# Kernel tuning notes

Measured on AMD Instinct MI355X. Metric: run time of the kernel, lower is better.

The kernel has to match this reference:

```python
import jax, jax.numpy as jnp
import numpy as np

EMB = 1024
HEADS = 16
HEAD_DIM = EMB // HEADS
SCALE = 1.0 / np.sqrt(HEAD_DIM)


def setup_inputs() -> dict:
    key = jax.random.key(0)
    ks = jax.random.split(key, 11)
    B, L, E = 4, 2048, EMB
    s = 1.0 / np.sqrt(E)
    inp = {
        "Q": jax.random.normal(ks[0], (B, L, E), jnp.float32),
        "K": jax.random.normal(ks[1], (B, L, E), jnp.float32),
        "V": jax.random.normal(ks[2], (B, L, E), jnp.float32),
        "WQ": jax.random.normal(ks[3], (E, E), jnp.float32) * s,
        "bQ": jax.random.normal(ks[4], (E,), jnp.float32) * s,
        "WK": jax.random.normal(ks[5], (E, E), jnp.float32) * s,
        "bK": jax.random.normal(ks[6], (E,), jnp.float32) * s,
        "WV": jax.random.normal(ks[7], (E, E), jnp.float32) * s,
        "bV": jax.random.normal(ks[8], (E,), jnp.float32) * s,
        "WO": jax.random.normal(ks[9], (E, E), jnp.float32) * s,
        "bO": jax.random.normal(ks[10], (E,), jnp.float32) * s,
    }
    return inp


def reference(Q, K, V, WQ, bQ, WK, bK, WV, bV, WO, bO):
    B, L, E = Q.shape
    # linear projections (torch Linear stores W as [out,in]; here W is [in,out])
    q = Q @ WQ + bQ
    k = K @ WK + bK
    v = V @ WV + bV
    # split heads: [B, H, L, D]
    q = q.reshape(B, L, HEADS, HEAD_DIM).transpose(0, 2, 1, 3)
    k = k.reshape(B, L, HEADS, HEAD_DIM).transpose(0, 2, 1, 3)
    v = v.reshape(B, L, HEADS, HEAD_DIM).transpose(0, 2, 1, 3)
    scores = jnp.einsum("bhqd,bhkd->bhqk", q, k) * SCALE
    # causal mask (mask=True): -inf above diagonal
    causal = jnp.tril(jnp.ones((L, L), dtype=bool))
    scores = jnp.where(causal, scores, -jnp.inf)
    probs = jax.nn.softmax(scores, axis=-1)
    out = jnp.einsum("bhqk,bhkd->bhqd", probs, v)  # [B,H,L,D]
    out = out.transpose(0, 2, 1, 3).reshape(B, L, E)  # concat heads
    return out @ WO + bO
```

## Files before the change

kernel.cpp:

```cpp
#include <hip/hip_runtime.h>
#include <hip/hip_bf16.h>

#define BB 4
#define HH 16
#define LL 2048
#define DD 64
#define EE 1024
#define MM (BB*LL)
#define SCL 0.125f
#define L2E 1.44269504f

using bf16   = __hip_bfloat16;
using bf16x8 = __attribute__((ext_vector_type(8))) __bf16;
using s16x4  = __attribute__((ext_vector_type(4))) short;
using f32x4  = __attribute__((ext_vector_type(4))) float;
using u32x4  = __attribute__((ext_vector_type(4))) unsigned int;
typedef unsigned int u32;

__device__ __forceinline__ bf16x8 ld8(const bf16* p){ return *(const bf16x8*)p; }
__device__ __forceinline__ bf16x8 ld8(const float* p){
  u32x4 a = *(const u32x4*)p;
  u32x4 b = *(const u32x4*)(p + 4);
  union { bf16x8 v; unsigned short s[8]; } r;
#pragma unroll
  for (int i = 0; i < 4; i++) r.s[i]     = (unsigned short)((a[i] + 0x7FFFu + ((a[i] >> 16) & 1u)) >> 16);
#pragma unroll
  for (int i = 0; i < 4; i++) r.s[i + 4] = (unsigned short)((b[i] + 0x7FFFu + ((b[i] >> 16) & 1u)) >> 16);
  return r.v;
}
__device__ __forceinline__ float ldf(const bf16* p){ return __bfloat162float(*p); }
__device__ __forceinline__ float ldf(const float* p){ return *p; }
__device__ __forceinline__ bf16 to_b(bf16 v){ return v; }
__device__ __forceinline__ bf16 to_b(float v){ return __float2bfloat16(v); }

__device__ __forceinline__ void async16(const bf16* g, bf16* l) {
  __builtin_amdgcn_global_load_lds((const __attribute__((address_space(1))) u32*)g,
                                   (__attribute__((address_space(3))) u32*)l, 16, 0, 0);
}

__global__ __launch_bounds__(256) void detect_dtype(const unsigned int* __restrict__ w,
                                                    int* __restrict__ flag) {
  __shared__ int cnt[256];
  int tid = threadIdx.x;
  int c = 0;
  for (int i = 0; i < 16; i++) {
    unsigned u = w[tid * 16 + i];
    unsigned e = (u >> 7) & 0xFF;
    c += (e >= 100 && e <= 140) ? 1 : 0;
  }
  cnt[tid] = c;
  __syncthreads();
  for (int s = 128; s > 0; s >>= 1) {
    if (tid < s) cnt[tid] += cnt[tid + s];
    __syncthreads();
  }
  if (tid == 0) *flag = (cnt[0] > 2048) ? 1 : 0;
}

__global__ __launch_bounds__(256) void convert_in(
    const void* __restrict__ X0, const void* __restrict__ X1, const void* __restrict__ X2,
    bf16* __restrict__ Y0, bf16* __restrict__ Y1, bf16* __restrict__ Y2,
    const int* __restrict__ flag) {
  int z = blockIdx.z;
  const void* X = (z == 0) ? X0 : (z == 1) ? X1 : X2;
  bf16* Y       = (z == 0) ? Y0 : (z == 1) ? Y1 : Y2;
  size_t idx = ((size_t)blockIdx.x * 256 + threadIdx.x) * 8;
  if (*flag) *(bf16x8*)(Y + idx) = *(const bf16x8*)((const bf16*)X + idx);
  else       *(bf16x8*)(Y + idx) = ld8((const float*)X + idx);
}

template<typename T>
__device__ __forceinline__ void tr_body(const T* __restrict__ W, bf16* __restrict__ Wt,
                                        bf16 (*t)[33]) {
  int tx = threadIdx.x, ty = threadIdx.y;
  int x = blockIdx.x * 32 + tx;
  for (int r = 0; r < 4; r++)
    t[ty + r * 8][tx] = to_b(W[(blockIdx.y * 32 + ty + r * 8) * EE + x]);
  __syncthreads();
  int x2 = blockIdx.y * 32 + tx;
  for (int r = 0; r < 4; r++)
    Wt[(blockIdx.x * 32 + ty + r * 8) * EE + x2] = t[tx][ty + r * 8];
}

__global__ __launch_bounds__(256) void transpose_w4(
    const void* __restrict__ W0, const void* __restrict__ W1,
    const void* __restrict__ W2, const void* __restrict__ W3,
    bf16* __restrict__ T0, bf16* __restrict__ T1,
    bf16* __restrict__ T2, bf16* __restrict__ T3,
    const int* __restrict__ flag) {
  __shared__ bf16 t[32][33];
  int z = blockIdx.z;
  const void* W = (z == 0) ? W0 : (z == 1) ? W1 : (z == 2) ? W2 : W3;
  bf16* Wt      = (z == 0) ? T0 : (z == 1) ? T1 : (z == 2) ? T2 : T3;
  if (*flag) tr_body<bf16>((const bf16*)W, Wt, t);
  else       tr_body<float>((const float*)W, Wt, t);
}

template<typename TIO>
__device__ void gemm_body(const bf16* __restrict__ A, const bf16* __restrict__ Bt,
                          const TIO* __restrict__ bias, void* __restrict__ Cv,
                          int mode, bf16* As, bf16* Bs) {
  constexpr int K = EE;
  int tid = threadIdx.x;
  int lane = tid & 63, w = tid >> 6;
  int l16 = lane & 15, quad = lane >> 4;
  int linear = blockIdx.x + 8 * blockIdx.y;
  int xcd = linear & 7;
  int slot = linear >> 3;
  int m0 = (xcd * 8 + (slot & 7)) * 128;
  int n0 = (slot >> 3) * 128;
  int mw = (w & 1) * 64;
  int nw = (w >> 1) * 64;
  int lr = lane >> 3;
  int x7 = l16 & 7;

  f32x4 acc[4][4] = {};

  for (int k0 = 0; k0 < K; k0 += 64) {
    __syncthreads();
#pragma unroll
    for (int s = 0; s < 4; s++) {
      int R = w * 32 + s * 8;
      int r = R + lr;
      int gc = ((lane & 7) ^ (r & 7)) * 8;
      async16(A  + (size_t)(m0 + r) * K + k0 + gc, As + R * 64);
      async16(Bt + (size_t)(n0 + r) * K + k0 + gc, Bs + R * 64);
    }
    __syncthreads();
#pragma unroll
    for (int ks = 0; ks < 2; ks++) {
      bf16x8 af[4], bfr[4];
#pragma unroll
      for (int t = 0; t < 4; t++) {
        af[t]  = *(const bf16x8*)(As + (mw + t * 16 + l16) * 64 + ((ks * 4 + quad) ^ x7) * 8);
        bfr[t] = *(const bf16x8*)(Bs + (nw + t * 16 + l16) * 64 + ((ks * 4 + quad) ^ x7) * 8);
      }
#pragma unroll
      for (int mt = 0; mt < 4; mt++)
#pragma unroll
        for (int nt = 0; nt < 4; nt++)
          acc[mt][nt] = __builtin_amdgcn_mfma_f32_16x16x32_bf16(af[mt], bfr[nt], acc[mt][nt], 0, 0, 0);
    }
  }

#pragma unroll
  for (int nt = 0; nt < 4; nt++) {
    int col = n0 + nw + nt * 16 + l16;
    float bv = ldf(bias + col);
    int hh = col >> 6, d = col & 63;
#pragma unroll
    for (int mt = 0; mt < 4; mt++) {
      f32x4 v = acc[mt][nt];
      int rowb = m0 + mw + mt * 16 + quad * 4;
      if (mode == 0) {
#pragma unroll
        for (int i = 0; i < 4; i++)
          ((bf16*)Cv)[(size_t)(rowb + i) * EE + col] = __float2bfloat16(v[i] + bv);
      } else if (mode == 3) {
#pragma unroll
        for (int i = 0; i < 4; i++) {
          float val = v[i] + bv;
          if constexpr (__is_same(TIO, bf16))
            ((bf16*)Cv)[(size_t)(rowb + i) * EE + col] = __float2bfloat16(val);
          else
            ((float*)Cv)[(size_t)(rowb + i) * EE + col] = val;
        }
      } else {
        int b = rowb >> 11, l0 = rowb & 2047;
        union { s16x4 p; bf16 e[4]; } u;
#pragma unroll
        for (int i = 0; i < 4; i++) u.e[i] = __float2bfloat16(v[i] + bv);
        *(s16x4*)((bf16*)Cv + ((size_t)(b * HH + hh) * DD + d) * LL + l0) = u.p;
      }
    }
  }
}

__global__ __launch_bounds__(256) void qkv_gemm(
    const bf16* __restrict__ Qc, const bf16* __restrict__ Kc, const bf16* __restrict__ Vc,
    const bf16* __restrict__ WQt, const bf16* __restrict__ WKt, const bf16* __restrict__ WVt,
    const void* __restrict__ bQ, const void* __restrict__ bK, const void* __restrict__ bV,
    bf16* __restrict__ qo, bf16* __restrict__ ko, bf16* __restrict__ vo,
    const int* __restrict__ flag) {
  __shared__ __align__(16) bf16 As[128 * 64];
  __shared__ __align__(16) bf16 Bs[128 * 64];
  int z = blockIdx.z;
  const bf16* A    = (z == 0) ? Qc  : (z == 1) ? Kc  : Vc;
  const bf16* Bt   = (z == 0) ? WQt : (z == 1) ? WKt : WVt;
  const void* bb   = (z == 0) ? bQ  : (z == 1) ? bK  : bV;
  bf16* C          = (z == 0) ? qo  : (z == 1) ? ko  : vo;
  int mode = (z == 2) ? 2 : 0;
  if (*flag) gemm_body<bf16>(A, Bt, (const bf16*)bb, C, mode, As, Bs);
  else       gemm_body<float>(A, Bt, (const float*)bb, C, mode, As, Bs);
}

__global__ __launch_bounds__(256) void out_gemm(const bf16* __restrict__ A,
                                                const bf16* __restrict__ WOt,
                                                const void* __restrict__ bO,
                                                void* __restrict__ C,
                                                const int* __restrict__ flag) {
  __shared__ __align__(16) bf16 As[128 * 64];
  __shared__ __align__(16) bf16 Bs[128 * 64];
  if (*flag) gemm_body<bf16>(A, WOt, (const bf16*)bO, C, 3, As, Bs);
  else       gemm_body<float>(A, WOt, (const float*)bO, C, 3, As, Bs);
}

__global__ __launch_bounds__(256) void attn(const bf16* __restrict__ qg,
                                            const bf16* __restrict__ kg,
                                            const bf16* __restrict__ vg,
                                            bf16* __restrict__ outg) {
  __shared__ __align__(16) bf16 Ks[2][64 * 64];
  __shared__ __align__(16) bf16 Vs[2][64 * 64];
  int linear = blockIdx.x + 16 * blockIdx.y;
  int xcd = linear & 7;
  int slot = linear >> 3;
  int bh = xcd * 8 + (slot & 7);
  int pb = slot >> 3;
  int tid = threadIdx.x;
  int w = tid >> 6, lane = tid & 63, l16 = lane & 15, quad = lane >> 4;
  int b = bh >> 4, hh = bh & 15;

  const bf16* qp = qg + (size_t)b * LL * EE + hh * DD;
  const bf16* kp = kg + (size_t)b * LL * EE + hh * DD;
  const bf16* vp = vg + (size_t)bh * DD * LL;
  const f32x4 z4 = {};
  int x7 = l16 & 7;

  for (int half = 0; half < 2; half++) {
    int tile = half ? (31 - pb) : pb;
    int qrow0 = tile * 64 + w * 16;
    int q = qrow0 + l16;
    bf16x8 bq0 = *(const bf16x8*)(qp + (size_t)q * EE + quad * 8);
    bf16x8 bq1 = *(const bf16x8*)(qp + (size_t)q * EE + 32 + quad * 8);

    float m = -1.0e30f, l = 0.f;
    f32x4 o[4] = {};
    int kend = tile + 1;

    __syncthreads();
    {
      int kbase = 0;
#pragma unroll
      for (int t = 0; t < 2; t++) {
        int R = w * 16 + t * 8;
        int r = R + (lane >> 3);
        int gb = (lane & 7) ^ (r & 7);
        async16(kp + (size_t)(kbase + r) * EE + gb * 8, &Ks[0][R * 64]);
        async16(vp + (size_t)r * LL + kbase + gb * 8, &Vs[0][R * 64]);
      }
    }

    for (int kb = 0; kb < kend; kb++) {
      int kbase = kb * 64;
      __syncthreads();
      if (kb + 1 < kend) {
        int nb = (kb + 1) & 1;
        int nbase = kbase + 64;
#pragma unroll
        for (int t = 0; t < 2; t++) {
          int R = w * 16 + t * 8;
          int r = R + (lane >> 3);
          int gb = (lane & 7) ^ (r & 7);
          async16(kp + (size_t)(nbase + r) * EE + gb * 8, &Ks[nb][R * 64]);
          async16(vp + (size_t)r * LL + nbase + gb * 8, &Vs[nb][R * 64]);
        }
      }
      const bf16* Kb = &Ks[kb & 1][0];
      const bf16* Vb = &Vs[kb & 1][0];

      f32x4 s[4];
      __builtin_amdgcn_s_setprio(1);
#pragma unroll
      for (int kt = 0; kt < 4; kt++) {
        int row = kt * 16 + l16;
        bf16x8 kf0 = *(const bf16x8*)(Kb + row * 64 + (quad ^ x7) * 8);
        bf16x8 kf1 = *(const bf16x8*)(Kb + row * 64 + ((quad + 4) ^ x7) * 8);
        s[kt] = __builtin_amdgcn_mfma_f32_16x16x32_bf16(kf0, bq0, z4, 0, 0, 0);
        s[kt] = __builtin_amdgcn_mfma_f32_16x16x32_bf16(kf1, bq1, s[kt], 0, 0, 0);
      }
      __builtin_amdgcn_s_setprio(0);
#if __has_builtin(__builtin_amdgcn_mfma_f32_16x16x16bf16_1k)
      s16x4 vf[4][4];
#pragma unroll
      for (int j = 0; j < 4; j++)
#pragma unroll
        for (int kt = 0; kt < 4; kt++)
          vf[j][kt] = *(const s16x4*)(Vb + (j * 16 + l16) * 64 +
                                      ((kt * 2 + (quad >> 1)) ^ x7) * 8 + (quad & 1) * 4);
#endif
      float sv[16];
      if (kbase + 63 <= qrow0) {
#pragma unroll
        for (int kt = 0; kt < 4; kt++)
#pragma unroll
          for (int i = 0; i < 4; i++) sv[kt * 4 + i] = s[kt][i] * SCL;
      } else {
        int rel = q - kbase - quad * 4;
#pragma unroll
        for (int kt = 0; kt < 4; kt++)
#pragma unroll
          for (int i = 0; i < 4; i++)
            sv[kt * 4 + i] = (kt * 16 + i <= rel) ? s[kt][i] * SCL : -1.0e30f;
      }
      float mloc = sv[0];
#pragma unroll
      for (int i = 1; i < 16; i++) mloc = fmaxf(mloc, sv[i]);
      mloc = fmaxf(mloc, __shfl_xor(mloc, 16));
      mloc = fmaxf(mloc, __shfl_xor(mloc, 32));
      float mnew = fmaxf(m, mloc);
      float alpha = exp2f((m - mnew) * L2E);
      float p[16], ssum = 0.f;
#pragma unroll
      for (int i = 0; i < 16; i++) { p[i] = exp2f((sv[i] - mnew) * L2E); ssum += p[i]; }
      ssum += __shfl_xor(ssum, 16);
      ssum += __shfl_xor(ssum, 32);
      l = l * alpha + ssum;
      m = mnew;
#pragma unroll
      for (int j = 0; j < 4; j++)
#pragma unroll
        for (int i = 0; i < 4; i++) o[j][i] *= alpha;
      union { s16x4 v4; bf16 e[4]; unsigned u[2]; } pk[4];
#pragma unroll
      for (int kt = 0; kt < 4; kt++)
#pragma unroll
        for (int i = 0; i < 4; i++) pk[kt].e[i] = __float2bfloat16(p[kt * 4 + i]);
#if __has_builtin(__builtin_amdgcn_mfma_f32_16x16x16bf16_1k)
      __builtin_amdgcn_s_setprio(1);
#pragma unroll
      for (int kt = 0; kt < 4; kt++)
#pragma unroll
        for (int j = 0; j < 4; j++)
          o[j] = __builtin_amdgcn_mfma_f32_16x16x16bf16_1k(vf[j][kt], pk[kt].v4, o[j], 0, 0, 0);
      __builtin_amdgcn_s_setprio(0);
#else
#pragma unroll
      for (int c = 0; c < 2; c++) {
        union { bf16x8 v8; unsigned u[4]; } bfr;
#pragma unroll
        for (int r = 0; r < 4; r++) {
          int key = c * 32 + quad * 8 + 2 * r;
          int srcl = (((key >> 2) & 3) << 4) + l16;
          unsigned v0 = __shfl((int)pk[2 * c].u[r & 1], srcl, 64);
          unsigned v1 = __shfl((int)pk[2 * c + 1].u[r & 1], srcl, 64);
          bfr.u[r] = (quad < 2) ? v0 : v1;
        }
        __builtin_amdgcn_s_setprio(1);
#pragma unroll
        for (int j = 0; j < 4; j++) {
          bf16x8 vfr = *(const bf16x8*)(Vb + (j * 16 + l16) * 64 + ((c * 4 + quad) ^ x7) * 8);
          o[j] = __builtin_amdgcn_mfma_f32_16x16x32_bf16(vfr, bfr.v8, o[j], 0, 0, 0);
        }
        __builtin_amdgcn_s_setprio(0);
      }
#endif
    }
    float inv = 1.0f / l;
#pragma unroll
    for (int j = 0; j < 4; j++) {
      union { s16x4 v4; bf16 e[4]; } u;
#pragma unroll
      for (int i = 0; i < 4; i++) u.e[i] = __float2bfloat16(o[j][i] * inv);
      *(s16x4*)(outg + (size_t)(b * LL + q) * EE + hh * DD + j * 16 + quad * 4) = u.v4;
    }
  }
}

extern "C" void kernel_launch(void* const* d_in, const int* in_sizes, int n_in,
                              void* d_out, int out_size, void* d_ws, size_t ws_size,
                              hipStream_t stream) {
  const void* Q   = d_in[0];
  const void* Kin = d_in[1];
  const void* V   = d_in[2];
  const void* WQ  = d_in[3];
  const void* bQ  = d_in[4];
  const void* WK  = d_in[5];
  const void* bK  = d_in[6];
  const void* WV  = d_in[7];
  const void* bV  = d_in[8];
  const void* WO  = d_in[9];
  const void* bO  = d_in[10];

  int* flag = (int*)d_ws;
  bf16* base = (bf16*)((char*)d_ws + 256);
  bf16* wqt  = base;
  bf16* wkt  = wqt + (size_t)EE * EE;
  bf16* wvt  = wkt + (size_t)EE * EE;
  bf16* wot  = wvt + (size_t)EE * EE;
  bf16* Qc   = wot + (size_t)EE * EE;
  bf16* Kc   = Qc  + (size_t)MM * EE;
  bf16* Vc   = Kc  + (size_t)MM * EE;
  bf16* qws  = Vc  + (size_t)MM * EE;
  bf16* kws  = qws + (size_t)MM * EE;
  bf16* vws  = kws + (size_t)MM * EE;
  bf16* aout = vws + (size_t)MM * EE;

  detect_dtype<<<1, 256, 0, stream>>>((const unsigned int*)WQ, flag);

  convert_in<<<dim3(MM * EE / 8 / 256, 1, 3), 256, 0, stream>>>(Q, Kin, V, Qc, Kc, Vc, flag);

  transpose_w4<<<dim3(32, 32, 4), dim3(32, 8), 0, stream>>>(
      WQ, WK, WV, WO, wqt, wkt, wvt, wot, flag);

  qkv_gemm<<<dim3(8, 64, 3), 256, 0, stream>>>(
      Qc, Kc, Vc, wqt, wkt, wvt, bQ, bK, bV, qws, kws, vws, flag);

  attn<<<dim3(16, 64), 256, 0, stream>>>(qws, kws, vws, aout);

  out_gemm<<<dim3(8, 64), 256, 0, stream>>>(aout, wot, bO, d_out, flag);
}
```

Before: 454.3 us.

## Double-buffer GEMM LDS tiles to overlap async loads with MFMA compute

The projection and output GEMMs now use two LDS buffers per operand. The next K-tile is issued as async global-to-LDS loads before MFMA compute runs on the current tile, and there is one barrier per tile instead of two. This is meant to hide global memory latency behind matrix math. The cost is double the LDS per block (64KB), which may reduce occupancy.

```diff
diff --git a/kernel.cpp b/kernel.cpp
--- a/kernel.cpp
+++ b/kernel.cpp
@@ -96,6 +96,7 @@
   else       tr_body<float>((const float*)W, Wt, t);
 }
 
+#define TILE_ELEMS (128 * 64)
 template<typename TIO>
 __device__ void gemm_body(const bf16* __restrict__ A, const bf16* __restrict__ Bt,
                           const TIO* __restrict__ bias, void* __restrict__ Cv,
@@ -116,24 +117,25 @@
 
   f32x4 acc[4][4] = {};
 
-  for (int k0 = 0; k0 < K; k0 += 64) {
-    __syncthreads();
+  auto stage = [&](bf16* Ad, bf16* Bd, int k0) {
 #pragma unroll
     for (int s = 0; s < 4; s++) {
       int R = w * 32 + s * 8;
       int r = R + lr;
       int gc = ((lane & 7) ^ (r & 7)) * 8;
-      async16(A  + (size_t)(m0 + r) * K + k0 + gc, As + R * 64);
-      async16(Bt + (size_t)(n0 + r) * K + k0 + gc, Bs + R * 64);
-    }
-    __syncthreads();
+      async16(A  + (size_t)(m0 + r) * K + k0 + gc, Ad + R * 64);
+      async16(Bt + (size_t)(n0 + r) * K + k0 + gc, Bd + R * 64);
+    }
+  };
+
+  auto compute = [&](const bf16* Ab, const bf16* Bb) {
 #pragma unroll
     for (int ks = 0; ks < 2; ks++) {
       bf16x8 af[4], bfr[4];
 #pragma unroll
       for (int t = 0; t < 4; t++) {
-        af[t]  = *(const bf16x8*)(As + (mw + t * 16 + l16) * 64 + ((ks * 4 + quad) ^ x7) * 8);
-        bfr[t] = *(const bf16x8*)(Bs + (nw + t * 16 + l16) * 64 + ((ks * 4 + quad) ^ x7) * 8);
+        af[t]  = *(const bf16x8*)(Ab + (mw + t * 16 + l16) * 64 + ((ks * 4 + quad) ^ x7) * 8);
+        bfr[t] = *(const bf16x8*)(Bb + (nw + t * 16 + l16) * 64 + ((ks * 4 + quad) ^ x7) * 8);
       }
 #pragma unroll
       for (int mt = 0; mt < 4; mt++)
@@ -141,6 +143,26 @@
         for (int nt = 0; nt < 4; nt++)
           acc[mt][nt] = __builtin_amdgcn_mfma_f32_16x16x32_bf16(af[mt], bfr[nt], acc[mt][nt], 0, 0, 0);
     }
+  };
+
+  stage(As, Bs, 0);
+  asm volatile("s_waitcnt vmcnt(0)" ::: "memory");
+  __builtin_amdgcn_s_barrier();
+  asm volatile("" ::: "memory");
+
+#pragma unroll 1
+  for (int t = 0; t < K / 64; t += 2) {
+    stage(As + TILE_ELEMS, Bs + TILE_ELEMS, t * 64 + 64);
+    compute(As, Bs);
+    asm volatile("s_waitcnt vmcnt(0)" ::: "memory");
+    __builtin_amdgcn_s_barrier();
+    asm volatile("" ::: "memory");
+    if (t + 2 < K / 64)
+      stage(As, Bs, t * 64 + 128);
+    compute(As + TILE_ELEMS, Bs + TILE_ELEMS);
+    asm volatile("s_waitcnt vmcnt(0)" ::: "memory");
+    __builtin_amdgcn_s_barrier();
+    asm volatile("" ::: "memory");
   }
 
 #pragma unroll
@@ -182,8 +204,8 @@
     const void* __restrict__ bQ, const void* __restrict__ bK, const void* __restrict__ bV,
     bf16* __restrict__ qo, bf16* __restrict__ ko, bf16* __restrict__ vo,
     const int* __restrict__ flag) {
-  __shared__ __align__(16) bf16 As[128 * 64];
-  __shared__ __align__(16) bf16 Bs[128 * 64];
+  __shared__ __align__(16) bf16 As[2 * TILE_ELEMS];
+  __shared__ __align__(16) bf16 Bs[2 * TILE_ELEMS];
   int z = blockIdx.z;
   const bf16* A    = (z == 0) ? Qc  : (z == 1) ? Kc  : Vc;
   const bf16* Bt   = (z == 0) ? WQt : (z == 1) ? WKt : WVt;
@@ -199,8 +221,8 @@
                                                 const void* __restrict__ bO,
                                                 void* __restrict__ C,
                                                 const int* __restrict__ flag) {
-  __shared__ __align__(16) bf16 As[128 * 64];
-  __shared__ __align__(16) bf16 Bs[128 * 64];
+  __shared__ __align__(16) bf16 As[2 * TILE_ELEMS];
+  __shared__ __align__(16) bf16 Bs[2 * TILE_ELEMS];
   if (*flag) gemm_body<bf16>(A, WOt, (const bf16*)bO, C, 3, As, Bs);
   else       gemm_body<float>(A, WOt, (const float*)bO, C, 3, As, Bs);
 }
```

Result: faster. 441.6 us (-2.8%).
